# Performance work log

Measured on AMD Instinct MI355X. Metric: run time of the kernel, lower is better.

Reference implementation:

```python
import jax, jax.numpy as jnp
import numpy as np

N_NODES = 20000
N_EDGES = 320000
INDIM = 64
OUTDIM = 128
EDGE_DIM = 16
HEADS = 4
ED = OUTDIM // 2          # encoded edge dim = 64
C1 = 2 * INDIM // HEADS   # 32 -> concat 128
C2 = OUTDIM // HEADS      # 32 -> concat 128
C3 = 2 * OUTDIM // HEADS  # 64 -> concat 256


def setup_inputs() -> dict:
    key = jax.random.key(0)
    ks = iter(jax.random.split(key, 80))
    def p(*shape):
        return jax.random.normal(next(ks), shape, dtype=jnp.float32) * 0.05
    inp = {}
    inp['x_in'] = jax.random.normal(next(ks), (N_NODES, INDIM), dtype=jnp.float32)
    inp['edge_index'] = jax.random.randint(next(ks), (2, N_EDGES), 0, N_NODES)
    inp['edge_attr'] = jax.random.normal(next(ks), (N_EDGES, EDGE_DIM), dtype=jnp.float32)
    # BatchNorm1d (eval mode: running stats)
    inp['bn0_g'] = jnp.ones(INDIM, jnp.float32) + p(INDIM)
    inp['bn0_b'] = p(INDIM)
    inp['bn0_m'] = p(INDIM)
    inp['bn0_v'] = jnp.ones(INDIM, jnp.float32) + 0.1 * jax.random.uniform(next(ks), (INDIM,))
    # edge encoder: Linear(edge_dim,outdim) -> LeakyReLU -> Linear(outdim,outdim//2) -> LeakyReLU
    inp['ee_W1'] = p(EDGE_DIM, OUTDIM); inp['ee_b1'] = p(OUTDIM)
    inp['ee_W2'] = p(OUTDIM, ED); inp['ee_b2'] = p(ED)
    # GATv2 layers: lin_l, lin_r (bias), lin_edge (no bias), att [H,C], out bias [H*C]
    def gat_params(prefix, din, C):
        inp[prefix + '_Wl'] = p(din, HEADS * C); inp[prefix + '_bl'] = p(HEADS * C)
        inp[prefix + '_Wr'] = p(din, HEADS * C); inp[prefix + '_br'] = p(HEADS * C)
        inp[prefix + '_We'] = p(ED, HEADS * C)
        inp[prefix + '_att'] = p(HEADS, C)
        inp[prefix + '_bias'] = p(HEADS * C)
    gat_params('g1', INDIM, C1)
    gat_params('g2', HEADS * C1, C2)
    gat_params('g3', HEADS * C2, C3)
    # LayerNorms
    inp['ln1_g'] = jnp.ones(HEADS * C1, jnp.float32); inp['ln1_b'] = p(HEADS * C1)
    inp['ln2_g'] = jnp.ones(HEADS * C2, jnp.float32); inp['ln2_b'] = p(HEADS * C2)
    inp['ln3_g'] = jnp.ones(HEADS * C3, jnp.float32); inp['ln3_b'] = p(HEADS * C3)
    # skip / mixing / heads
    inp['skip_W'] = p(INDIM, HEADS * C1); inp['skip_b'] = p(HEADS * C1)
    inp['alpha_p'] = jnp.float32(0.3)
    inp['fp_W'] = p(HEADS * C1, HEADS * C3); inp['fp_b'] = p(HEADS * C3)
    catout = HEADS * C3
    inp['np_W1'] = p(catout, catout // 2); inp['np_b1'] = p(catout // 2)
    inp['np_W2'] = p(catout // 2, catout // 4); inp['np_b2'] = p(catout // 4)
    inp['np_W3'] = p(catout // 4, 1); inp['np_b3'] = p(1)
    return inp


def _ln(x, g, b):
    m = jnp.mean(x, axis=-1, keepdims=True)
    v = jnp.var(x, axis=-1, keepdims=True)
    return (x - m) / jnp.sqrt(v + 1e-5) * g + b


def _gatv2(x, src, dst, ea, Wl, bl, Wr, br, We, att, bias, N):
    # GATv2Conv (eval): e = att . leaky_relu(x_j + x_i + e_ij, 0.2); segment softmax over dst
    H, C = att.shape
    xl = (x @ Wl + bl).reshape(N, H, C)   # source transform
    xr = (x @ Wr + br).reshape(N, H, C)   # target transform
    ee = (ea @ We).reshape(-1, H, C)      # edge transform (no bias)
    m = jax.nn.leaky_relu(xl[src] + xr[dst] + ee, 0.2)  # [E,H,C]
    e = jnp.einsum('ehc,hc->eh', m, att)
    emax = jax.ops.segment_max(e, dst, num_segments=N)
    ex = jnp.exp(e - emax[dst])
    den = jax.ops.segment_sum(ex, dst, num_segments=N)
    alpha = ex / (den[dst] + 1e-16)       # [E,H]
    out = jax.ops.segment_sum(xl[src] * alpha[:, :, None], dst, num_segments=N)
    return out.reshape(N, H * C) + bias, alpha


def reference(x_in, edge_index, edge_attr, bn0_g, bn0_b, bn0_m, bn0_v,
              ee_W1, ee_b1, ee_W2, ee_b2,
              g1_Wl, g1_bl, g1_Wr, g1_br, g1_We, g1_att, g1_bias,
              g2_Wl, g2_bl, g2_Wr, g2_br, g2_We, g2_att, g2_bias,
              g3_Wl, g3_bl, g3_Wr, g3_br, g3_We, g3_att, g3_bias,
              ln1_g, ln1_b, ln2_g, ln2_b, ln3_g, ln3_b,
              skip_W, skip_b, alpha_p, fp_W, fp_b,
              np_W1, np_b1, np_W2, np_b2, np_W3, np_b3):
    N = x_in.shape[0]
    # BatchNorm1d eval
    x = (x_in - bn0_m) / jnp.sqrt(bn0_v + 1e-5) * bn0_g + bn0_b
    # edge encoder + L2 normalize
    ea = jax.nn.leaky_relu(edge_attr @ ee_W1 + ee_b1, 0.01)
    ea = jax.nn.leaky_relu(ea @ ee_W2 + ee_b2, 0.01)
    ea = ea / jnp.maximum(jnp.linalg.norm(ea, axis=-1, keepdims=True), 1e-12)
    # add self loops (fill_value='mean' of incoming encoded edge_attr)
    src0, dst0 = edge_index[0], edge_index[1]
    deg = jax.ops.segment_sum(jnp.ones_like(ea[:, 0]), dst0, num_segments=N)
    loop_attr = jax.ops.segment_sum(ea, dst0, num_segments=N) / jnp.maximum(deg, 1.0)[:, None]
    ar = jnp.arange(N, dtype=src0.dtype)
    src = jnp.concatenate([src0, ar]); dst = jnp.concatenate([dst0, ar])
    ea2 = jnp.concatenate([ea, loop_attr], axis=0)
    x1, a1 = _gatv2(x, src, dst, ea2, g1_Wl, g1_bl, g1_Wr, g1_br, g1_We, g1_att, g1_bias, N)
    x1 = jax.nn.leaky_relu(_ln(x1, ln1_g, ln1_b), 0.01)
    skip1 = 0.01 * (x @ skip_W + skip_b) + x1  # skip_weight = 0.01 (frozen)
    x2, a2 = _gatv2(skip1, src, dst, ea2, g2_Wl, g2_bl, g2_Wr, g2_br, g2_We, g2_att, g2_bias, N)
    x2 = jax.nn.leaky_relu(_ln(x2, ln2_g, ln2_b), 0.01)
    x3, a3 = _gatv2(x2, src, dst, ea2, g3_Wl, g3_bl, g3_Wr, g3_br, g3_We, g3_att, g3_bias, N)
    x3 = jax.nn.leaky_relu(_ln(x3, ln3_g, ln3_b), 0.01)
    s = jax.nn.sigmoid(alpha_p)
    xf = s * (x1 @ fp_W + fp_b) + (1.0 - s) * x3
    h = jax.nn.elu(xf @ np_W1 + np_b1)
    h = jax.nn.elu(h @ np_W2 + np_b2)
    node_probs = h @ np_W3 + np_b3
    return (xf, node_probs, a1, a2, a3)
```

## Files before the change

### kernel.cpp

```cpp
#include <hip/hip_runtime.h>
#include <math.h>

#define DEV __device__ __forceinline__

typedef __attribute__((ext_vector_type(8))) short bf16x8;
typedef __attribute__((ext_vector_type(4))) float f32x4;

DEV float leakyf(float x, float s) { return x > 0.f ? x : s * x; }

DEV unsigned short f2bf(float f) {
  unsigned u = __float_as_uint(f);
  unsigned r = (u + 0x7fff + ((u >> 16) & 1)) >> 16;
  return (unsigned short)r;
}
DEV float bf2f(unsigned short h) { return __uint_as_float((unsigned)h << 16); }

DEV float sel4(float4 v, int h) {
  float a = (h & 1) ? v.y : v.x;
  float b = (h & 1) ? v.w : v.z;
  return (h & 2) ? b : a;
}

DEV float wave_sum(float v) {
#pragma unroll
  for (int o = 1; o < 64; o <<= 1) v += __shfl_xor(v, o);
  return v;
}
DEV float wave_max(float v) {
#pragma unroll
  for (int o = 1; o < 64; o <<= 1) v = fmaxf(v, __shfl_xor(v, o));
  return v;
}

struct WJob { const float* in; unsigned short* out; int K; int Nc; };
struct WJobs { WJob j[13]; };

__global__ __launch_bounds__(256) void wt_kernel(WJobs jobs) {
  WJob jb = jobs.j[blockIdx.y];
  int total = jb.K * jb.Nc;
  for (int i = blockIdx.x * 256 + threadIdx.x; i < total; i += gridDim.x * 256) {
    int c = i / jb.K, k = i - c * jb.K;
    jb.out[i] = f2bf(jb.in[(size_t)k * jb.Nc + c]);
  }
}

__global__ __launch_bounds__(256) void bn_kernel(
    const float* __restrict__ xin, const float* __restrict__ g,
    const float* __restrict__ b, const float* __restrict__ m,
    const float* __restrict__ v, float* __restrict__ xout, int total) {
  int i = blockIdx.x * 256 + threadIdx.x;
  if (i < total) {
    int c = i & 63;
    xout[i] = (xin[i] - m[c]) * rsqrtf(v[c] + 1e-5f) * g[c] + b[c];
  }
}

__global__ __launch_bounds__(256, 2) void edge_enc_kernel(
    const float* __restrict__ edge_attr, const unsigned short* __restrict__ WT1,
    const float* __restrict__ b1, const unsigned short* __restrict__ WT2,
    const float* __restrict__ b2, unsigned short* __restrict__ ea_csr,
    const int* __restrict__ inv, int E) {
  __shared__ unsigned short sEa1[64][136];
  int tid = threadIdx.x, lane = tid & 63, w = tid >> 6;
  int g = lane >> 4, q = lane & 15;
  bf16x8 w1f[8];
#pragma unroll
  for (int t = 0; t < 8; t++) {
    bf16x8 v = {};
    if (g < 2) v = *(const bf16x8*)(WT1 + (size_t)(16 * t + q) * 16 + 8 * g);
    w1f[t] = v;
  }
  float b1v[8];
#pragma unroll
  for (int t = 0; t < 8; t++) b1v[t] = b1[16 * t + q];
  bf16x8 w2f[4][4];
#pragma unroll
  for (int t = 0; t < 4; t++)
#pragma unroll
    for (int kc = 0; kc < 4; kc++)
      w2f[t][kc] = *(const bf16x8*)(WT2 + (size_t)(16 * t + q) * 128 + 32 * kc + 8 * g);
  float b2v[4];
#pragma unroll
  for (int t = 0; t < 4; t++) b2v[t] = b2[16 * t + q];

  int gstride = gridDim.x * 64;

  auto load_attr = [&](int base) -> bf16x8 {
    bf16x8 af = {};
    if (g < 2) {
      int e = base + w * 16 + q;
      if (e >= E) e = E - 1;
      const float* ap = edge_attr + (size_t)e * 16 + 8 * g;
      float4 x0 = *(const float4*)ap;
      float4 x1 = *(const float4*)(ap + 4);
      af[0] = (short)f2bf(x0.x); af[1] = (short)f2bf(x0.y);
      af[2] = (short)f2bf(x0.z); af[3] = (short)f2bf(x0.w);
      af[4] = (short)f2bf(x1.x); af[5] = (short)f2bf(x1.y);
      af[6] = (short)f2bf(x1.z); af[7] = (short)f2bf(x1.w);
    }
    return af;
  };

  int base = blockIdx.x * 64;
  if (base >= E) return;
  bf16x8 af = load_attr(base);
  for (; base < E; ) {
    int next = base + gstride;
    bf16x8 af_next = {};
    if (next < E) af_next = load_attr(next);
    int e0 = base + w * 16;
    f32x4 acc1[8];
#pragma unroll
    for (int t = 0; t < 8; t++) acc1[t] = (f32x4){0.f, 0.f, 0.f, 0.f};
#pragma unroll
    for (int t = 0; t < 8; t++)
      acc1[t] = __builtin_amdgcn_mfma_f32_16x16x32_bf16(af, w1f[t], acc1[t], 0, 0, 0);
#pragma unroll
    for (int t = 0; t < 8; t++)
#pragma unroll
      for (int r = 0; r < 4; r++) {
        float v = leakyf(acc1[t][r] + b1v[t], 0.01f);
        sEa1[w * 16 + g * 4 + r][16 * t + q] = f2bf(v);
      }
    f32x4 acc2[4];
#pragma unroll
    for (int t = 0; t < 4; t++) acc2[t] = (f32x4){0.f, 0.f, 0.f, 0.f};
#pragma unroll
    for (int kc = 0; kc < 4; kc++) {
      bf16x8 a2 = *(const bf16x8*)&sEa1[w * 16 + q][32 * kc + 8 * g];
#pragma unroll
      for (int t = 0; t < 4; t++)
        acc2[t] = __builtin_amdgcn_mfma_f32_16x16x32_bf16(a2, w2f[t][kc], acc2[t], 0, 0, 0);
    }
#pragma unroll
    for (int r = 0; r < 4; r++) {
      float vv[4];
      float p = 0.f;
#pragma unroll
      for (int t = 0; t < 4; t++) {
        float v = leakyf(acc2[t][r] + b2v[t], 0.01f);
        vv[t] = v;
        p += v * v;
      }
#pragma unroll
      for (int o = 1; o < 16; o <<= 1) p += __shfl_xor(p, o);
      float sc = 1.f / fmaxf(sqrtf(p), 1e-12f);
      int e = e0 + g * 4 + r;
      if (e < E) {
        int pos = inv[e];
#pragma unroll
        for (int t = 0; t < 4; t++)
          ea_csr[(size_t)pos * 64 + 16 * t + q] = f2bf(vv[t] * sc);
      }
    }
    af = af_next;
    base = next;
  }
}

__global__ __launch_bounds__(256) void count_kernel(const int* __restrict__ dst0,
                                                    int* __restrict__ counts, int E, int E2) {
  int i = blockIdx.x * 256 + threadIdx.x;
  if (i < E2) {
    int d = (i < E) ? dst0[i] : (i - E);
    atomicAdd(&counts[d], 1);
  }
}

__global__ __launch_bounds__(1024) void scan_kernel(const int* __restrict__ counts,
                                                    int* __restrict__ rowptr,
                                                    int* __restrict__ fill, int N) {
  __shared__ int part[1024];
  int tid = threadIdx.x;
  int chunk = (N + 1023) / 1024;
  int lo = tid * chunk, hi = lo + chunk;
  if (hi > N) hi = N;
  if (lo > N) lo = N;
  int s = 0;
  for (int i = lo; i < hi; i++) s += counts[i];
  part[tid] = s;
  __syncthreads();
#pragma unroll
  for (int o = 1; o < 1024; o <<= 1) {
    int v = (tid >= o) ? part[tid - o] : 0;
    __syncthreads();
    part[tid] += v;
    __syncthreads();
  }
  if (tid == 1023) rowptr[N] = part[1023];
  int off = part[tid] - s;
  for (int i = lo; i < hi; i++) {
    rowptr[i] = off;
    fill[i] = off;
    off += counts[i];
  }
}

__global__ __launch_bounds__(256) void fill_kernel(const int* __restrict__ src0,
                                                   const int* __restrict__ dst0,
                                                   int* __restrict__ fill,
                                                   int* __restrict__ csr,
                                                   int* __restrict__ srcpos,
                                                   int* __restrict__ dstpos,
                                                   int* __restrict__ inv, int E, int E2) {
  int i = blockIdx.x * 256 + threadIdx.x;
  if (i < E2) {
    int d, s;
    if (i < E) {
      d = dst0[i];
      s = src0[i];
    } else {
      d = s = i - E;
    }
    int pos = atomicAdd(&fill[d], 1);
    csr[pos] = i;
    srcpos[pos] = s;
    dstpos[pos] = d;
    inv[i] = pos;
  }
}

__global__ __launch_bounds__(256) void loopattr_kernel(unsigned short* __restrict__ ea_csr,
                                                       const int* __restrict__ rowptr,
                                                       const int* __restrict__ csr, int N, int E) {
  int lane = threadIdx.x & 63, wv = threadIdx.x >> 6;
  int stride = gridDim.x * 4;
  for (int n = blockIdx.x * 4 + wv; n < N; n += stride) {
    int r0 = rowptr[n], r1 = rowptr[n + 1];
    float acc = 0.f;
    int loop_pos = r0;
    for (int i = r0; i < r1; i++) {
      int e = csr[i];
      if (e < E) {
        acc += bf2f(ea_csr[(size_t)i * 64 + lane]);
      } else {
        loop_pos = i;
      }
    }
    int cnt = r1 - r0 - 1;
    ea_csr[(size_t)loop_pos * 64 + lane] = f2bf(acc / fmaxf((float)cnt, 1.f));
  }
}

template <int MODE>
__global__ __launch_bounds__(256) void gemm_mfma_kernel(
    const float* __restrict__ A, const unsigned short* __restrict__ BT,
    const float* __restrict__ bias, void* __restrict__ Cout, int M, int K, int Nc,
    const float* __restrict__ aux, const float* __restrict__ alpha_p) {
  __shared__ unsigned short sA[64][40];
  __shared__ unsigned short sB[64][40];
  int tid = threadIdx.x, lane = tid & 63, w = tid >> 6;
  int g = lane >> 4, q = lane & 15;
  int bm = blockIdx.y * 64, bn = blockIdx.x * 64;
  f32x4 acc[4];
#pragma unroll
  for (int t = 0; t < 4; t++) acc[t] = (f32x4){0.f, 0.f, 0.f, 0.f};
  int r = tid >> 2, ko = (tid & 3) * 8;
  for (int k0 = 0; k0 < K; k0 += 32) {
    {
      int gm = bm + r;
      bf16x8 v = {};
      if (gm < M) {
        const float* ap = A + (size_t)gm * K + k0 + ko;
        float4 x0 = *(const float4*)ap;
        float4 x1 = *(const float4*)(ap + 4);
        v[0] = (short)f2bf(x0.x); v[1] = (short)f2bf(x0.y);
        v[2] = (short)f2bf(x0.z); v[3] = (short)f2bf(x0.w);
        v[4] = (short)f2bf(x1.x); v[5] = (short)f2bf(x1.y);
        v[6] = (short)f2bf(x1.z); v[7] = (short)f2bf(x1.w);
      }
      *(bf16x8*)&sA[r][ko] = v;
      int gc = bn + r;
      bf16x8 bv = {};
      if (gc < Nc) bv = *(const bf16x8*)(BT + (size_t)gc * K + k0 + ko);
      *(bf16x8*)&sB[r][ko] = bv;
    }
    __syncthreads();
    bf16x8 a = *(const bf16x8*)&sA[w * 16 + q][8 * g];
#pragma unroll
    for (int t = 0; t < 4; t++) {
      bf16x8 b = *(const bf16x8*)&sB[16 * t + q][8 * g];
      acc[t] = __builtin_amdgcn_mfma_f32_16x16x32_bf16(a, b, acc[t], 0, 0, 0);
    }
    __syncthreads();
  }
  float s = 0.f;
  if (MODE == 3) s = 1.f / (1.f + __expf(-alpha_p[0]));
#pragma unroll
  for (int t = 0; t < 4; t++) {
    int col = bn + 16 * t + q;
#pragma unroll
    for (int rr = 0; rr < 4; rr++) {
      int row = bm + w * 16 + g * 4 + rr;
      if (row < M && col < Nc) {
        float v = acc[t][rr] + bias[col];
        if (MODE == 2) v = v > 0.f ? v : (__expf(v) - 1.f);
        if (MODE == 3) v = s * v + (1.f - s) * aux[(size_t)row * Nc + col];
        if (MODE == 1)
          ((unsigned short*)Cout)[(size_t)row * Nc + col] = f2bf(v);
        else
          ((float*)Cout)[(size_t)row * Nc + col] = v;
      }
    }
  }
}

struct GJob { const unsigned short* BT; const float* bias; void* out; int mode; };
struct GJobs { GJob j[3]; };

__global__ __launch_bounds__(256) void gemm_mfma_batched(
    const float* __restrict__ A, GJobs jobs, int M, int K, int Nc) {
  __shared__ unsigned short sA[64][40];
  __shared__ unsigned short sB[64][40];
  GJob jb = jobs.j[blockIdx.z];
  const unsigned short* BT = jb.BT;
  int tid = threadIdx.x, lane = tid & 63, w = tid >> 6;
  int g = lane >> 4, q = lane & 15;
  int bm = blockIdx.y * 64, bn = blockIdx.x * 64;
  f32x4 acc[4];
#pragma unroll
  for (int t = 0; t < 4; t++) acc[t] = (f32x4){0.f, 0.f, 0.f, 0.f};
  int r = tid >> 2, ko = (tid & 3) * 8;
  for (int k0 = 0; k0 < K; k0 += 32) {
    {
      int gm = bm + r;
      bf16x8 v = {};
      if (gm < M) {
        const float* ap = A + (size_t)gm * K + k0 + ko;
        float4 x0 = *(const float4*)ap;
        float4 x1 = *(const float4*)(ap + 4);
        v[0] = (short)f2bf(x0.x); v[1] = (short)f2bf(x0.y);
        v[2] = (short)f2bf(x0.z); v[3] = (short)f2bf(x0.w);
        v[4] = (short)f2bf(x1.x); v[5] = (short)f2bf(x1.y);
        v[6] = (short)f2bf(x1.z); v[7] = (short)f2bf(x1.w);
      }
      *(bf16x8*)&sA[r][ko] = v;
      int gc = bn + r;
      bf16x8 bv = {};
      if (gc < Nc) bv = *(const bf16x8*)(BT + (size_t)gc * K + k0 + ko);
      *(bf16x8*)&sB[r][ko] = bv;
    }
    __syncthreads();
    bf16x8 a = *(const bf16x8*)&sA[w * 16 + q][8 * g];
#pragma unroll
    for (int t = 0; t < 4; t++) {
      bf16x8 b = *(const bf16x8*)&sB[16 * t + q][8 * g];
      acc[t] = __builtin_amdgcn_mfma_f32_16x16x32_bf16(a, b, acc[t], 0, 0, 0);
    }
    __syncthreads();
  }
#pragma unroll
  for (int t = 0; t < 4; t++) {
    int col = bn + 16 * t + q;
#pragma unroll
    for (int rr = 0; rr < 4; rr++) {
      int row = bm + w * 16 + g * 4 + rr;
      if (row < M && col < Nc) {
        float v = acc[t][rr] + jb.bias[col];
        if (jb.mode == 1)
          ((unsigned short*)jb.out)[(size_t)row * Nc + col] = f2bf(v);
        else
          ((float*)jb.out)[(size_t)row * Nc + col] = v;
      }
    }
  }
}

template <int C, bool SPLIT>
__global__ __launch_bounds__(256) void score_mfma_kernel(
    const unsigned short* __restrict__ ea_csr, const unsigned short* __restrict__ xl,
    const unsigned short* __restrict__ xr, const float* __restrict__ We,
    const float* __restrict__ att, const int* __restrict__ srcpos,
    const int* __restrict__ dstpos,
    float* __restrict__ e_s, int E2, int HCfull, int col_off_in) {
  int lane = threadIdx.x & 63;
  int wv = threadIdx.x >> 6;
  int g = lane >> 4, q = lane & 15;
  int col_off = SPLIT ? (wv & 1) * 128 : col_off_in;
  bf16x8 bfrag[8][2];
#pragma unroll
  for (int t = 0; t < 8; t++)
#pragma unroll
    for (int kc = 0; kc < 2; kc++) {
      bf16x8 bv;
#pragma unroll
      for (int j = 0; j < 8; j++) {
        int k = kc * 32 + g * 8 + j;
        bv[j] = (short)f2bf(We[(size_t)k * HCfull + col_off + 16 * t + q]);
      }
      bfrag[t][kc] = bv;
    }
  float attv[8];
#pragma unroll
  for (int t = 0; t < 8; t++) attv[t] = att[col_off + 16 * t + q];

  constexpr int TPH = C / 16;
  constexpr int NH = 8 / TPH;
  const int headbase = col_off / C;

  int tiles = (E2 + 15) / 16;
  int tstart = SPLIT ? (blockIdx.x * 2 + (wv >> 1)) : (blockIdx.x * 4 + wv);
  int nw = SPLIT ? (gridDim.x * 2) : (gridDim.x * 4);
  for (int tile = tstart; tile < tiles; tile += nw) {
    int i0 = tile * 16;
    int ia = i0 + q;
    if (ia >= E2) ia = E2 - 1;
    const unsigned short* ap = ea_csr + (size_t)ia * 64 + g * 8;
    bf16x8 a0 = *(const bf16x8*)(ap);
    bf16x8 a1 = *(const bf16x8*)(ap + 32);
    f32x4 acc[8];
#pragma unroll
    for (int t = 0; t < 8; t++) acc[t] = (f32x4){0.f, 0.f, 0.f, 0.f};
#pragma unroll
    for (int t = 0; t < 8; t++) {
      acc[t] = __builtin_amdgcn_mfma_f32_16x16x32_bf16(a0, bfrag[t][0], acc[t], 0, 0, 0);
      acc[t] = __builtin_amdgcn_mfma_f32_16x16x32_bf16(a1, bfrag[t][1], acc[t], 0, 0, 0);
    }
    int sn[4], dn[4];
#pragma unroll
    for (int r = 0; r < 4; r++) {
      int i = i0 + g * 4 + r;
      if (i >= E2) i = E2 - 1;
      sn[r] = srcpos[i];
      dn[r] = dstpos[i];
    }
    float p[NH][4];
#pragma unroll
    for (int hh = 0; hh < NH; hh++)
#pragma unroll
      for (int r = 0; r < 4; r++) p[hh][r] = 0.f;
#pragma unroll
    for (int t = 0; t < 8; t++) {
      int col = col_off + 16 * t + q;
#pragma unroll
      for (int r = 0; r < 4; r++) {
        float xv = bf2f(xl[(size_t)sn[r] * HCfull + col]) +
                   bf2f(xr[(size_t)dn[r] * HCfull + col]) + acc[t][r];
        xv = xv > 0.f ? xv : 0.2f * xv;
        p[t / TPH][r] += xv * attv[t];
      }
    }
#pragma unroll
    for (int hh = 0; hh < NH; hh++)
#pragma unroll
      for (int r = 0; r < 4; r++) {
#pragma unroll
        for (int o = 1; o < 16; o <<= 1) p[hh][r] += __shfl_xor(p[hh][r], o);
      }
    if (q == 0) {
#pragma unroll
      for (int r = 0; r < 4; r++) {
        int i = i0 + g * 4 + r;
        if (i < E2) {
#pragma unroll
          for (int hh = 0; hh < NH; hh++)
            e_s[(size_t)i * 4 + headbase + hh] = p[hh][r];
        }
      }
    }
  }
}

template <int HC, bool L1MODE>
__global__ __launch_bounds__(256) void aggr_kernel(
    const float* __restrict__ e_s, const unsigned short* __restrict__ xl,
    const int* __restrict__ rowptr, const int* __restrict__ srcpos,
    const float* __restrict__ bias,
    const float* __restrict__ lng, const float* __restrict__ lnb,
    float* __restrict__ xout,
    float* __restrict__ x1out, const float* __restrict__ skipproj,
    float* __restrict__ md, int N) {
  constexpr int CPL = HC / 64;
  int lane = threadIdx.x & 63, wv = threadIdx.x >> 6;
  int stride = gridDim.x * 4;
  const float4* e_s4 = (const float4*)e_s;
  for (int n = blockIdx.x * 4 + wv; n < N; n += stride) {
    int r0 = rowptr[n], r1 = rowptr[n + 1];
    float m0 = -1e30f, m1 = -1e30f, m2 = -1e30f, m3 = -1e30f;
    for (int i = r0 + lane; i < r1; i += 64) {
      float4 v = e_s4[i];
      m0 = fmaxf(m0, v.x);
      m1 = fmaxf(m1, v.y);
      m2 = fmaxf(m2, v.z);
      m3 = fmaxf(m3, v.w);
    }
    m0 = wave_max(m0);
    m1 = wave_max(m1);
    m2 = wave_max(m2);
    m3 = wave_max(m3);
    float d0 = 0.f, d1 = 0.f, d2 = 0.f, d3 = 0.f;
    for (int i = r0 + lane; i < r1; i += 64) {
      float4 v = e_s4[i];
      d0 += __expf(v.x - m0);
      d1 += __expf(v.y - m1);
      d2 += __expf(v.z - m2);
      d3 += __expf(v.w - m3);
    }
    d0 = wave_sum(d0);
    d1 = wave_sum(d1);
    d2 = wave_sum(d2);
    d3 = wave_sum(d3);
    float i0 = 1.f / (d0 + 1e-16f), i1 = 1.f / (d1 + 1e-16f);
    float i2 = 1.f / (d2 + 1e-16f), i3 = 1.f / (d3 + 1e-16f);
    if (lane == 0) {
      float* mp = md + (size_t)n * 8;
      mp[0] = m0; mp[1] = m1; mp[2] = m2; mp[3] = m3;
      mp[4] = i0; mp[5] = i1; mp[6] = i2; mp[7] = i3;
    }
    int h = lane >> 4;
    float mh = (h & 2) ? ((h & 1) ? m3 : m2) : ((h & 1) ? m1 : m0);
    float ih = (h & 2) ? ((h & 1) ? i3 : i2) : ((h & 1) ? i1 : i0);
    float acc[CPL];
#pragma unroll
    for (int j = 0; j < CPL; j++) acc[j] = 0.f;
    int c0 = lane * CPL;
    int i = r0;
    for (; i + 4 <= r1; i += 4) {
      float sh0, sh1, sh2, sh3;
      int sn0, sn1, sn2, sn3;
      {
        float4 a = e_s4[i], b = e_s4[i + 1], c = e_s4[i + 2], d = e_s4[i + 3];
        sh0 = sel4(a, h); sh1 = sel4(b, h); sh2 = sel4(c, h); sh3 = sel4(d, h);
      }
      sn0 = srcpos[i]; sn1 = srcpos[i + 1]; sn2 = srcpos[i + 2]; sn3 = srcpos[i + 3];
      if constexpr (CPL == 2) {
        ushort2 t0 = *(const ushort2*)(xl + (size_t)sn0 * HC + c0);
        ushort2 t1 = *(const ushort2*)(xl + (size_t)sn1 * HC + c0);
        ushort2 t2 = *(const ushort2*)(xl + (size_t)sn2 * HC + c0);
        ushort2 t3 = *(const ushort2*)(xl + (size_t)sn3 * HC + c0);
        float a0 = __expf(sh0 - mh) * ih;
        float a1 = __expf(sh1 - mh) * ih;
        float a2 = __expf(sh2 - mh) * ih;
        float a3 = __expf(sh3 - mh) * ih;
        acc[0] += a0 * bf2f(t0.x) + a1 * bf2f(t1.x) + a2 * bf2f(t2.x) + a3 * bf2f(t3.x);
        acc[1] += a0 * bf2f(t0.y) + a1 * bf2f(t1.y) + a2 * bf2f(t2.y) + a3 * bf2f(t3.y);
      } else {
        ushort4 t0 = *(const ushort4*)(xl + (size_t)sn0 * HC + c0);
        ushort4 t1 = *(const ushort4*)(xl + (size_t)sn1 * HC + c0);
        ushort4 t2 = *(const ushort4*)(xl + (size_t)sn2 * HC + c0);
        ushort4 t3 = *(const ushort4*)(xl + (size_t)sn3 * HC + c0);
        float a0 = __expf(sh0 - mh) * ih;
        float a1 = __expf(sh1 - mh) * ih;
        float a2 = __expf(sh2 - mh) * ih;
        float a3 = __expf(sh3 - mh) * ih;
        acc[0] += a0 * bf2f(t0.x) + a1 * bf2f(t1.x) + a2 * bf2f(t2.x) + a3 * bf2f(t3.x);
        acc[1] += a0 * bf2f(t0.y) + a1 * bf2f(t1.y) + a2 * bf2f(t2.y) + a3 * bf2f(t3.y);
        acc[2] += a0 * bf2f(t0.z) + a1 * bf2f(t1.z) + a2 * bf2f(t2.z) + a3 * bf2f(t3.z);
        acc[3] += a0 * bf2f(t0.w) + a1 * bf2f(t1.w) + a2 * bf2f(t2.w) + a3 * bf2f(t3.w);
      }
    }
    for (; i < r1; i++) {
      float sh = sel4(e_s4[i], h);
      float a = __expf(sh - mh) * ih;
      int sn = srcpos[i];
      const unsigned short* xp = xl + (size_t)sn * HC + c0;
      if constexpr (CPL == 2) {
        ushort2 t = *(const ushort2*)xp;
        acc[0] += a * bf2f(t.x);
        acc[1] += a * bf2f(t.y);
      } else {
        ushort4 t = *(const ushort4*)xp;
        acc[0] += a * bf2f(t.x);
        acc[1] += a * bf2f(t.y);
        acc[2] += a * bf2f(t.z);
        acc[3] += a * bf2f(t.w);
      }
    }
    float vals[CPL];
    float vs = 0.f, vq = 0.f;
#pragma unroll
    for (int j = 0; j < CPL; j++) {
      float t = acc[j] + bias[c0 + j];
      vals[j] = t;
      vs += t;
      vq += t * t;
    }
    vs = wave_sum(vs);
    vq = wave_sum(vq);
    float mean = vs * (1.f / HC);
    float var = vq * (1.f / HC) - mean * mean;
    float rstd = rsqrtf(fmaxf(var, 0.f) + 1e-5f);
#pragma unroll
    for (int j = 0; j < CPL; j++) {
      int c = c0 + j;
      float y = (vals[j] - mean) * rstd * lng[c] + lnb[c];
      y = leakyf(y, 0.01f);
      if constexpr (L1MODE) {
        x1out[(size_t)n * HC + c] = y;
        xout[(size_t)n * HC + c] = 0.01f * skipproj[(size_t)n * HC + c] + y;
      } else {
        xout[(size_t)n * HC + c] = y;
      }
    }
  }
}

__global__ __launch_bounds__(256) void alpha_kernel(
    const float* __restrict__ e_s, const int* __restrict__ csr,
    const int* __restrict__ dstpos, const float* __restrict__ md,
    float* __restrict__ alpha_out, int E2) {
  int i = blockIdx.x * 256 + threadIdx.x;
  if (i < E2) {
    float4 sv = ((const float4*)e_s)[i];
    int d = dstpos[i];
    const float* mp = md + (size_t)d * 8;
    float4 a;
    a.x = __expf(sv.x - mp[0]) * mp[4];
    a.y = __expf(sv.y - mp[1]) * mp[5];
    a.z = __expf(sv.z - mp[2]) * mp[6];
    a.w = __expf(sv.w - mp[3]) * mp[7];
    ((float4*)alpha_out)[csr[i]] = a;
  }
}

extern "C" void kernel_launch(void* const* d_in, const int* in_sizes, int n_in,
                              void* d_out, int out_size, void* d_ws, size_t ws_size,
                              hipStream_t stream) {
  (void)n_in;
  (void)out_size;
  (void)ws_size;
  const float* x_in = (const float*)d_in[0];
  const int* edge_index = (const int*)d_in[1];
  const float* edge_attr = (const float*)d_in[2];
  const float* bn0_g = (const float*)d_in[3];
  const float* bn0_b = (const float*)d_in[4];
  const float* bn0_m = (const float*)d_in[5];
  const float* bn0_v = (const float*)d_in[6];
  const float* eeW1 = (const float*)d_in[7];
  const float* eeb1 = (const float*)d_in[8];
  const float* eeW2 = (const float*)d_in[9];
  const float* eeb2 = (const float*)d_in[10];
  const float* g1_Wl = (const float*)d_in[11];
  const float* g1_bl = (const float*)d_in[12];
  const float* g1_Wr = (const float*)d_in[13];
  const float* g1_br = (const float*)d_in[14];
  const float* g1_We = (const float*)d_in[15];
  const float* g1_att = (const float*)d_in[16];
  const float* g1_bias = (const float*)d_in[17];
  const float* g2_Wl = (const float*)d_in[18];
  const float* g2_bl = (const float*)d_in[19];
  const float* g2_Wr = (const float*)d_in[20];
  const float* g2_br = (const float*)d_in[21];
  const float* g2_We = (const float*)d_in[22];
  const float* g2_att = (const float*)d_in[23];
  const float* g2_bias = (const float*)d_in[24];
  const float* g3_Wl = (const float*)d_in[25];
  const float* g3_bl = (const float*)d_in[26];
  const float* g3_Wr = (const float*)d_in[27];
  const float* g3_br = (const float*)d_in[28];
  const float* g3_We = (const float*)d_in[29];
  const float* g3_att = (const float*)d_in[30];
  const float* g3_bias = (const float*)d_in[31];
  const float* ln1_g = (const float*)d_in[32];
  const float* ln1_b = (const float*)d_in[33];
  const float* ln2_g = (const float*)d_in[34];
  const float* ln2_b = (const float*)d_in[35];
  const float* ln3_g = (const float*)d_in[36];
  const float* ln3_b = (const float*)d_in[37];
  const float* skip_W = (const float*)d_in[38];
  const float* skip_b = (const float*)d_in[39];
  const float* alpha_p = (const float*)d_in[40];
  const float* fp_W = (const float*)d_in[41];
  const float* fp_b = (const float*)d_in[42];
  const float* np_W1 = (const float*)d_in[43];
  const float* np_b1 = (const float*)d_in[44];
  const float* np_W2 = (const float*)d_in[45];
  const float* np_b2 = (const float*)d_in[46];
  const float* np_W3 = (const float*)d_in[47];
  const float* np_b3 = (const float*)d_in[48];

  const int N = in_sizes[0] / 64;
  const int E = in_sizes[2] / 16;
  const int E2 = E + N;
  const int* src0 = edge_index;
  const int* dst0 = edge_index + E;

  float* ws = (float*)d_ws;
  size_t off = 0;
  float* x = ws + off;         off += (size_t)N * 64;
  unsigned short* ea_csr = (unsigned short*)(ws + off); off += (size_t)E2 * 32;
  unsigned short* xl = (unsigned short*)(ws + off);    off += (size_t)N * 128;
  unsigned short* xr = (unsigned short*)(ws + off);    off += (size_t)N * 128;
  float* skipproj = ws + off;  off += (size_t)N * 128;
  float* x1 = ws + off;        off += (size_t)N * 128;
  float* skip1 = ws + off;     off += (size_t)N * 128;
  float* x2 = ws + off;        off += (size_t)N * 128;
  float* x3 = ws + off;        off += (size_t)N * 256;
  float* e_s = ws + off;       off += (size_t)E2 * 4;
  float* h2 = ws + off;        off += (size_t)N * 64;
  float* md = ws + off;        off += (size_t)N * 8;
  int* counts = (int*)(ws + off);
  int* rowptr = counts + N;
  int* fill = rowptr + N + 1;
  int* csr = fill + N;
  int* srcpos = csr + E2;
  int* dstpos = srcpos + E2;
  int* inv = dstpos + E2;
  off += (size_t)(3 * N + 1 + 4 * E2);
  off = (off + 3) & ~(size_t)3;
  unsigned short* wtp = (unsigned short*)(ws + off);
  auto alloc_wt = [&](int elems) {
    unsigned short* p = wtp;
    wtp += (elems + 7) & ~7;
    return p;
  };
  unsigned short* wt_g1l = alloc_wt(64 * 128);
  unsigned short* wt_g1r = alloc_wt(64 * 128);
  unsigned short* wt_skip = alloc_wt(64 * 128);
  unsigned short* wt_g2l = alloc_wt(128 * 128);
  unsigned short* wt_g2r = alloc_wt(128 * 128);
  unsigned short* wt_g3l = alloc_wt(128 * 256);
  unsigned short* wt_g3r = alloc_wt(128 * 256);
  unsigned short* wt_fp = alloc_wt(128 * 256);
  unsigned short* wt_np1 = alloc_wt(256 * 128);
  unsigned short* wt_np2 = alloc_wt(128 * 64);
  unsigned short* wt_np3 = alloc_wt(64 * 1);
  unsigned short* wt_ee1 = alloc_wt(16 * 128);
  unsigned short* wt_ee2 = alloc_wt(128 * 64);

  float* out = (float*)d_out;
  float* xf = out;
  float* npout = out + (size_t)N * 256;
  float* a1 = npout + N;
  float* a2 = a1 + (size_t)E2 * 4;
  float* a3 = a2 + (size_t)E2 * 4;

  WJobs jobs;
  jobs.j[0] = {g1_Wl, wt_g1l, 64, 128};
  jobs.j[1] = {g1_Wr, wt_g1r, 64, 128};
  jobs.j[2] = {skip_W, wt_skip, 64, 128};
  jobs.j[3] = {g2_Wl, wt_g2l, 128, 128};
  jobs.j[4] = {g2_Wr, wt_g2r, 128, 128};
  jobs.j[5] = {g3_Wl, wt_g3l, 128, 256};
  jobs.j[6] = {g3_Wr, wt_g3r, 128, 256};
  jobs.j[7] = {fp_W, wt_fp, 128, 256};
  jobs.j[8] = {np_W1, wt_np1, 256, 128};
  jobs.j[9] = {np_W2, wt_np2, 128, 64};
  jobs.j[10] = {np_W3, wt_np3, 64, 1};
  jobs.j[11] = {eeW1, wt_ee1, 16, 128};
  jobs.j[12] = {eeW2, wt_ee2, 128, 64};

  hipMemsetAsync(counts, 0, (size_t)N * sizeof(int), stream);
  wt_kernel<<<dim3(64, 13), 256, 0, stream>>>(jobs);
  bn_kernel<<<(N * 64 + 255) / 256, 256, 0, stream>>>(x_in, bn0_g, bn0_b, bn0_m, bn0_v, x, N * 64);
  count_kernel<<<(E2 + 255) / 256, 256, 0, stream>>>(dst0, counts, E, E2);
  scan_kernel<<<1, 1024, 0, stream>>>(counts, rowptr, fill, N);
  fill_kernel<<<(E2 + 255) / 256, 256, 0, stream>>>(src0, dst0, fill, csr, srcpos, dstpos, inv, E, E2);
  edge_enc_kernel<<<1280, 256, 0, stream>>>(edge_attr, wt_ee1, eeb1, wt_ee2, eeb2, ea_csr, inv, E);
  loopattr_kernel<<<(N + 3) / 4, 256, 0, stream>>>(ea_csr, rowptr, csr, N, E);

  auto gemm = [&](int mode, const float* A, const unsigned short* BT, const float* bias,
                  void* Cp, int M, int K, int Nc, const float* aux) {
    dim3 gdim((Nc + 63) / 64, (M + 63) / 64);
    switch (mode) {
      case 0: gemm_mfma_kernel<0><<<gdim, 256, 0, stream>>>(A, BT, bias, Cp, M, K, Nc, nullptr, nullptr); break;
      case 2: gemm_mfma_kernel<2><<<gdim, 256, 0, stream>>>(A, BT, bias, Cp, M, K, Nc, nullptr, nullptr); break;
      case 3: gemm_mfma_kernel<3><<<gdim, 256, 0, stream>>>(A, BT, bias, Cp, M, K, Nc, aux, alpha_p); break;
    }
  };
  auto gemm_batch = [&](const float* A, int M, int K, int Nc, GJobs gj, int nz) {
    dim3 gdim((Nc + 63) / 64, (M + 63) / 64, nz);
    gemm_mfma_batched<<<gdim, 256, 0, stream>>>(A, gj, M, K, Nc);
  };

  const int nblk_node = (N + 3) / 4;
  const int score_blocks = 1024;
  const int nblk_edge = (E2 + 255) / 256;

  {
    GJobs gj;
    gj.j[0] = {wt_g1l, g1_bl, xl, 1};
    gj.j[1] = {wt_g1r, g1_br, xr, 1};
    gj.j[2] = {wt_skip, skip_b, skipproj, 0};
    gemm_batch(x, N, 64, 128, gj, 3);
  }
  score_mfma_kernel<32, false><<<score_blocks, 256, 0, stream>>>(ea_csr, xl, xr, g1_We, g1_att, srcpos, dstpos, e_s, E2, 128, 0);
  aggr_kernel<128, true><<<nblk_node, 256, 0, stream>>>(e_s, xl, rowptr, srcpos, g1_bias, ln1_g, ln1_b,
                                                        skip1, x1, skipproj, md, N);
  alpha_kernel<<<nblk_edge, 256, 0, stream>>>(e_s, csr, dstpos, md, a1, E2);
  {
    GJobs gj;
    gj.j[0] = {wt_g2l, g2_bl, xl, 1};
    gj.j[1] = {wt_g2r, g2_br, xr, 1};
    gj.j[2] = {nullptr, nullptr, nullptr, 0};
    gemm_batch(skip1, N, 128, 128, gj, 2);
  }
  score_mfma_kernel<32, false><<<score_blocks, 256, 0, stream>>>(ea_csr, xl, xr, g2_We, g2_att, srcpos, dstpos, e_s, E2, 128, 0);
  aggr_kernel<128, false><<<nblk_node, 256, 0, stream>>>(e_s, xl, rowptr, srcpos, g2_bias, ln2_g, ln2_b,
                                                         x2, nullptr, nullptr, md, N);
  alpha_kernel<<<nblk_edge, 256, 0, stream>>>(e_s, csr, dstpos, md, a2, E2);
  {
    GJobs gj;
    gj.j[0] = {wt_g3l, g3_bl, xl, 1};
    gj.j[1] = {wt_g3r, g3_br, xr, 1};
    gj.j[2] = {nullptr, nullptr, nullptr, 0};
    gemm_batch(x2, N, 128, 256, gj, 2);
  }
  score_mfma_kernel<64, true><<<score_blocks, 256, 0, stream>>>(ea_csr, xl, xr, g3_We, g3_att, srcpos, dstpos, e_s, E2, 256, 0);
  aggr_kernel<256, false><<<nblk_node, 256, 0, stream>>>(e_s, xl, rowptr, srcpos, g3_bias, ln3_g, ln3_b,
                                                         x3, nullptr, nullptr, md, N);
  alpha_kernel<<<nblk_edge, 256, 0, stream>>>(e_s, csr, dstpos, md, a3, E2);
  gemm(3, x1, wt_fp, fp_b, xf, N, 128, 256, x3);
  gemm(2, xf, wt_np1, np_b1, skipproj, N, 256, 128, nullptr);
  gemm(2, skipproj, wt_np2, np_b2, h2, N, 128, 64, nullptr);
  gemm(0, h2, wt_np3, np_b3, npout, N, 64, 1, nullptr);
}
```

Before: 505.9 us.

## Vectorize xl/xr gathers in score kernel via LDS transpose of MFMA output

The edge-score kernel now loads each lane's 8 contiguous bf16 features of xl and xr with one 16-byte vector load instead of 32 scalar 2-byte gathers per lane. The MFMA edge-projection results are written to shared memory and read back in the matching contiguous-column layout. This also shrinks the cross-lane head reduction to 2-3 shuffles. It aims to cut the gather-bound cost of the random per-edge reads, at the price of LDS traffic and a per-tile shared-memory round trip.

After: 508.8 us. No clear change (+0.6%).

```diff
diff --git a/kernel.cpp b/kernel.cpp
--- a/kernel.cpp
+++ b/kernel.cpp
@@ -373,6 +373,7 @@
     const float* __restrict__ att, const int* __restrict__ srcpos,
     const int* __restrict__ dstpos,
     float* __restrict__ e_s, int E2, int HCfull, int col_off_in) {
+  __shared__ float sEE[4][16][132];
   int lane = threadIdx.x & 63;
   int wv = threadIdx.x >> 6;
   int g = lane >> 4, q = lane & 15;
@@ -390,12 +391,9 @@
       }
       bfrag[t][kc] = bv;
     }
-  float attv[8];
-#pragma unroll
-  for (int t = 0; t < 8; t++) attv[t] = att[col_off + 16 * t + q];
-
-  constexpr int TPH = C / 16;
-  constexpr int NH = 8 / TPH;
+  float attv2[8];
+#pragma unroll
+  for (int j = 0; j < 8; j++) attv2[j] = att[col_off + 8 * q + j];
   const int headbase = col_off / C;
 
   int tiles = (E2 + 15) / 16;
@@ -424,38 +422,38 @@
       sn[r] = srcpos[i];
       dn[r] = dstpos[i];
     }
-    float p[NH][4];
-#pragma unroll
-    for (int hh = 0; hh < NH; hh++)
-#pragma unroll
-      for (int r = 0; r < 4; r++) p[hh][r] = 0.f;
-#pragma unroll
-    for (int t = 0; t < 8; t++) {
-      int col = col_off + 16 * t + q;
-#pragma unroll
-      for (int r = 0; r < 4; r++) {
-        float xv = bf2f(xl[(size_t)sn[r] * HCfull + col]) +
-                   bf2f(xr[(size_t)dn[r] * HCfull + col]) + acc[t][r];
-        xv = xv > 0.f ? xv : 0.2f * xv;
-        p[t / TPH][r] += xv * attv[t];
-      }
-    }
-#pragma unroll
-    for (int hh = 0; hh < NH; hh++)
-#pragma unroll
-      for (int r = 0; r < 4; r++) {
-#pragma unroll
-        for (int o = 1; o < 16; o <<= 1) p[hh][r] += __shfl_xor(p[hh][r], o);
-      }
-    if (q == 0) {
-#pragma unroll
-      for (int r = 0; r < 4; r++) {
-        int i = i0 + g * 4 + r;
-        if (i < E2) {
-#pragma unroll
-          for (int hh = 0; hh < NH; hh++)
-            e_s[(size_t)i * 4 + headbase + hh] = p[hh][r];
-        }
+    bf16x8 xlv[4], xrv[4];
+#pragma unroll
+    for (int r = 0; r < 4; r++) {
+      xlv[r] = *(const bf16x8*)(xl + (size_t)sn[r] * HCfull + col_off + 8 * q);
+      xrv[r] = *(const bf16x8*)(xr + (size_t)dn[r] * HCfull + col_off + 8 * q);
+    }
+#pragma unroll
+    for (int t = 0; t < 8; t++)
+#pragma unroll
+      for (int r = 0; r < 4; r++)
+        sEE[wv][g * 4 + r][16 * t + q] = acc[t][r];
+#pragma unroll
+    for (int r = 0; r < 4; r++) {
+      const float* eerow = &sEE[wv][g * 4 + r][8 * q];
+      float4 e0 = *(const float4*)(eerow);
+      float4 e1 = *(const float4*)(eerow + 4);
+      float ee[8] = {e0.x, e0.y, e0.z, e0.w, e1.x, e1.y, e1.z, e1.w};
+      float p = 0.f;
+#pragma unroll
+      for (int j = 0; j < 8; j++) {
+        float v = bf2f(xlv[r][j]) + bf2f(xrv[r][j]) + ee[j];
+        v = v > 0.f ? v : 0.2f * v;
+        p += v * attv2[j];
+      }
+      p += __shfl_xor(p, 1);
+      p += __shfl_xor(p, 2);
+      if (C == 64) p += __shfl_xor(p, 4);
+      int i = i0 + g * 4 + r;
+      if (C == 32) {
+        if ((q & 3) == 0 && i < E2) e_s[(size_t)i * 4 + headbase + (q >> 2)] = p;
+      } else {
+        if ((q & 7) == 0 && i < E2) e_s[(size_t)i * 4 + headbase + (q >> 3)] = p;
       }
     }
   }
```
